# Kernel optimization log

Hardware: AMD Instinct MI355X
Metric: run time of the kernel (lower is better)

The kernel has to match this reference:

```python
import jax, jax.numpy as jnp
import numpy as np

NEG = -1e30  # safe "log zero" that avoids -inf - -inf = nan


def _segment_logsumexp(vals, seg, num_seg):
    # vals: [A] arc scores, seg: [A] destination state ids -> [num_seg]
    m = jax.ops.segment_max(vals, seg, num_segments=num_seg)
    m = jnp.maximum(m, NEG)  # empty segments give -inf
    s = jax.ops.segment_sum(jnp.exp(vals - m[seg]), seg, num_segments=num_seg)
    return m + jnp.log(s + 1e-30)


def setup_inputs() -> dict:
    key = jax.random.key(0)
    ks = jax.random.split(key, 7)
    T, B, D = 150, 64, 2048
    S, A = 20000, 262144
    inp = {
        "input": jax.nn.log_softmax(
            jax.random.normal(ks[0], (T, B, D), dtype=jnp.float32), axis=-1
        ),
        "arc_logw": 0.1 * jax.random.normal(ks[1], (A,), dtype=jnp.float32),
        "init_logp": jax.nn.log_softmax(
            jax.random.normal(ks[2], (S,), dtype=jnp.float32)
        ),
        "final_logp": 0.1 * jax.random.normal(ks[3], (S,), dtype=jnp.float32),
        "from_state": jax.random.randint(ks[4], (A,), 0, S, dtype=jnp.int32),
        "to_state": jax.random.randint(ks[5], (A,), 0, S, dtype=jnp.int32),
        "pdf_id": jax.random.randint(ks[6], (A,), 0, D, dtype=jnp.int32),
    }
    return inp


def reference(input, arc_logw, init_logp, final_logp, from_state, to_state, pdf_id):
    # LF-MMI denominator objective: log-semiring forward recursion over the
    # denominator WFST, summed over the batch.
    T, B, D = input.shape
    S = init_logp.shape[0]

    def step(alpha, logp_t):
        # alpha: [B, S] log forward probs; logp_t: [B, D] frame log-likelihoods
        # arc score = alpha[from] + arc weight + nnet logprob of arc's pdf
        scores = alpha[:, from_state] + arc_logw[None, :] + logp_t[:, pdf_id]  # [B, A]
        new_alpha = jax.vmap(lambda v: _segment_logsumexp(v, to_state, S))(scores)
        return new_alpha, None

    alpha0 = jnp.broadcast_to(init_logp[None, :], (B, S))
    alphaT, _ = jax.lax.scan(step, alpha0, input)  # scan over T frames
    per_seq = jax.scipy.special.logsumexp(alphaT + final_logp[None, :], axis=-1)  # [B]
    return jnp.sum(per_seq)
```

## Files before the change

### kernel.cpp

```cpp
#include <hip/hip_runtime.h>
#include <hip/hip_bf16.h>
#include <hip/hip_fp16.h>

#define NEGV (-1e30f)

constexpr int Bc = 64;
constexpr int Dc = 2048;
constexpr int Tc = 150;
constexpr float DRIFT = -5.0f;
constexpr float CLAMP_LO = -60.0f, CLAMP_HI = 40.0f;

__global__ void transpose_kernel(const float* __restrict__ in, __half* __restrict__ out) {
    __shared__ float tile[64][65];
    const int t  = blockIdx.y;
    const int d0 = blockIdx.x * 64;
    const int lane = threadIdx.x & 63;
    const int w    = threadIdx.x >> 6;
    const float* inp = in + (size_t)t * Bc * Dc;
    #pragma unroll
    for (int b = w; b < 64; b += 4)
        tile[b][lane] = inp[(size_t)b * Dc + d0 + lane];
    __syncthreads();
    __half* outp = out + (size_t)t * Dc * Bc;
    #pragma unroll
    for (int d = w; d < 64; d += 4)
        outp[(size_t)(d0 + d) * Bc + lane] = __float2half(tile[lane][d]);
}

__global__ void init_alpha_kernel(const float* __restrict__ init_logp,
                                  __half* __restrict__ alpha_h, int S) {
    int idx  = blockIdx.x * blockDim.x + threadIdx.x;
    int wave = idx >> 6;
    int lane = threadIdx.x & 63;
    if (wave < S) {
        float v = fminf(fmaxf(init_logp[wave], CLAMP_LO), CLAMP_HI);
        alpha_h[(size_t)wave * Bc + lane] = __float2half(v);
    }
}

__global__ void hist_kernel(const int* __restrict__ to, int* __restrict__ count, int A) {
    int i = blockIdx.x * blockDim.x + threadIdx.x;
    if (i < A) atomicAdd(&count[to[i]], 1);
}

__global__ void scan_kernel(const int* __restrict__ count, int* __restrict__ row_ptr,
                            int* __restrict__ cursor, int S) {
    __shared__ int lds[1024];
    const int tid = threadIdx.x;
    const int n = 1024;
    const int chunk = (S + n - 1) / n;
    const int lo = tid * chunk;
    const int hi = min(lo + chunk, S);
    int local = 0;
    for (int j = lo; j < hi; ++j) local += count[j];
    lds[tid] = local;
    __syncthreads();
    for (int off = 1; off < 1024; off <<= 1) {
        int add = (tid >= off) ? lds[tid - off] : 0;
        __syncthreads();
        lds[tid] += add;
        __syncthreads();
    }
    int excl = (tid > 0) ? lds[tid - 1] : 0;
    for (int j = lo; j < hi; ++j) {
        int c = count[j];
        row_ptr[j] = excl;
        cursor[j]  = excl;
        excl += c;
    }
    if (tid == n - 1) row_ptr[S] = lds[n - 1];
}

__global__ void scatter_kernel(const int* __restrict__ to, const int* __restrict__ from,
                               const int* __restrict__ pdf, const float* __restrict__ w,
                               int* __restrict__ cursor, uint2* __restrict__ a_pack, int A) {
    int i = blockIdx.x * blockDim.x + threadIdx.x;
    if (i >= A) return;
    int t = to[i];
    int p = atomicAdd(&cursor[t], 1);
    unsigned short wb = __half_as_ushort(__float2half(w[i]));
    a_pack[p] = make_uint2((unsigned)from[i],
                           ((unsigned)pdf[i] & 0xffffu) | ((unsigned)wb << 16));
}

template <bool TR>
__global__ void step_kernel(const __half* __restrict__ alpha_old,
                            __half* __restrict__ alpha_new,
                            const float* __restrict__ off_old,
                            float* __restrict__ off_new,
                            const void* __restrict__ logp_t,
                            const int* __restrict__ row_ptr,
                            const uint2* __restrict__ arcs, int S) {
    const int nb  = gridDim.x;
    const int cpx = nb >> 3;
    const int bid = blockIdx.x;
    const int swz = (nb % 8 == 0) ? ((bid & 7) * cpx + (bid >> 3)) : bid;
    const int wave = (swz * blockDim.x + threadIdx.x) >> 6;
    const int lane = threadIdx.x & 63;
    if (wave >= S) return;
    const int lo = __builtin_amdgcn_readfirstlane(row_ptr[wave]);
    const int hi = __builtin_amdgcn_readfirstlane(row_ptr[wave + 1]);
    const __half* lph = (const __half*)logp_t;
    const float*  lpf = (const float*)logp_t;

    const float r0 = __half2float(alpha_old[0 * Bc + lane]);
    const float r1 = __half2float(alpha_old[1 * Bc + lane]);
    const float r2 = __half2float(alpha_old[2 * Bc + lane]);
    const float r3 = __half2float(alpha_old[3 * Bc + lane]);
    const float delta = fmaxf(fmaxf(r0, r1), fmaxf(r2, r3)) + DRIFT;

    float s0 = 0.0f, s1 = 0.0f, s2 = 0.0f, s3 = 0.0f;
    int i = lo;
    for (; i + 3 < hi; i += 4) {
        const uint2 A0 = arcs[i],     A1 = arcs[i + 1];
        const uint2 A2 = arcs[i + 2], A3 = arcs[i + 3];
        const float w0 = __half2float(__ushort_as_half((unsigned short)(A0.y >> 16)));
        const float w1 = __half2float(__ushort_as_half((unsigned short)(A1.y >> 16)));
        const float w2 = __half2float(__ushort_as_half((unsigned short)(A2.y >> 16)));
        const float w3 = __half2float(__ushort_as_half((unsigned short)(A3.y >> 16)));
        const float lp0 = TR ? __half2float(lph[(size_t)(A0.y & 0xffffu) * Bc + lane])
                             : lpf[(size_t)lane * Dc + (A0.y & 0xffffu)];
        const float lp1 = TR ? __half2float(lph[(size_t)(A1.y & 0xffffu) * Bc + lane])
                             : lpf[(size_t)lane * Dc + (A1.y & 0xffffu)];
        const float lp2 = TR ? __half2float(lph[(size_t)(A2.y & 0xffffu) * Bc + lane])
                             : lpf[(size_t)lane * Dc + (A2.y & 0xffffu)];
        const float lp3 = TR ? __half2float(lph[(size_t)(A3.y & 0xffffu) * Bc + lane])
                             : lpf[(size_t)lane * Dc + (A3.y & 0xffffu)];
        const float a0 = __half2float(alpha_old[(size_t)A0.x * Bc + lane]);
        const float a1 = __half2float(alpha_old[(size_t)A1.x * Bc + lane]);
        const float a2 = __half2float(alpha_old[(size_t)A2.x * Bc + lane]);
        const float a3 = __half2float(alpha_old[(size_t)A3.x * Bc + lane]);
        s0 += __expf(a0 + w0 + lp0);
        s1 += __expf(a1 + w1 + lp1);
        s2 += __expf(a2 + w2 + lp2);
        s3 += __expf(a3 + w3 + lp3);
    }
    for (; i < hi; ++i) {
        const uint2 A0 = arcs[i];
        const float w0 = __half2float(__ushort_as_half((unsigned short)(A0.y >> 16)));
        const float lp0 = TR ? __half2float(lph[(size_t)(A0.y & 0xffffu) * Bc + lane])
                             : lpf[(size_t)lane * Dc + (A0.y & 0xffffu)];
        s0 += __expf(__half2float(alpha_old[(size_t)A0.x * Bc + lane]) + w0 + lp0);
    }
    const float r = __logf(((s0 + s1) + (s2 + s3)) + 1e-30f);
    const float v = fminf(fmaxf(r - delta, CLAMP_LO), CLAMP_HI);
    alpha_new[(size_t)wave * Bc + lane] = __float2half(v);
    if (wave == 0) off_new[lane] = off_old[lane] + delta;
}

__global__ void final_reduce_kernel(const __half* __restrict__ alpha,
                                    const float* __restrict__ off,
                                    const float* __restrict__ final_logp,
                                    float* __restrict__ out, int S) {
    const int b = blockIdx.x;
    const int tid = threadIdx.x;
    float m = NEGV, sum = 0.0f;
    for (int s = tid; s < S; s += 256) {
        float v = __half2float(alpha[(size_t)s * Bc + b]) + final_logp[s];
        float nm = fmaxf(m, v);
        sum = sum * __expf(m - nm) + __expf(v - nm);
        m = nm;
    }
    __shared__ float mArr[256], sArr[256];
    mArr[tid] = m; sArr[tid] = sum;
    __syncthreads();
    for (int o = 128; o > 0; o >>= 1) {
        if (tid < o) {
            float m2 = mArr[tid + o], s2 = sArr[tid + o];
            float nm = fmaxf(mArr[tid], m2);
            sArr[tid] = sArr[tid] * __expf(mArr[tid] - nm) + s2 * __expf(m2 - nm);
            mArr[tid] = nm;
        }
        __syncthreads();
    }
    if (tid == 0) {
        float per = fmaxf(mArr[0], NEGV) + logf(sArr[0] + 1e-30f) + off[b];
        atomicAdd(out, per);
    }
}

extern "C" void kernel_launch(void* const* d_in, const int* in_sizes, int n_in,
                              void* d_out, int out_size, void* d_ws, size_t ws_size,
                              hipStream_t stream) {
    const float* input      = (const float*)d_in[0];
    const float* arc_logw   = (const float*)d_in[1];
    const float* init_logp  = (const float*)d_in[2];
    const float* final_logp = (const float*)d_in[3];
    const int*   from_state = (const int*)d_in[4];
    const int*   to_state   = (const int*)d_in[5];
    const int*   pdf_id     = (const int*)d_in[6];
    const int S = in_sizes[2];
    const int A = in_sizes[4];

    char* ws = (char*)d_ws;
    size_t off = 0;
    auto alloc = [&](size_t bytes) -> char* {
        char* p = ws + off;
        off += (bytes + 255) & ~(size_t)255;
        return p;
    };

    const size_t need_small =
        2 * (((size_t)S * Bc * 2 + 255) & ~(size_t)255) +
        (((size_t)A * 8 + 255) & ~(size_t)255) +
        3 * (((size_t)(S + 1) * 4 + 255) & ~(size_t)255) +
        2 * 256;
    const size_t need_T = (size_t)Tc * Dc * Bc * 2 + 256;
    const bool do_transpose = (ws_size >= need_small + need_T);

    __half* logpT = nullptr;
    if (do_transpose) logpT = (__half*)alloc(need_T);
    __half* alphaA = (__half*)alloc((size_t)S * Bc * 2);
    __half* alphaB = (__half*)alloc((size_t)S * Bc * 2);
    float* offA    = (float*)alloc(Bc * 4);
    float* offB    = (float*)alloc(Bc * 4);
    int*   row_ptr = (int*)alloc((size_t)(S + 1) * 4);
    int*   cursor  = (int*)alloc((size_t)(S + 1) * 4);
    int*   count   = (int*)alloc((size_t)(S + 1) * 4);
    uint2* a_pack  = (uint2*)alloc((size_t)A * 8);

    hipMemsetAsync(count, 0, (size_t)S * 4, stream);
    hipMemsetAsync(offA, 0, Bc * 4, stream);
    hipMemsetAsync(d_out, 0, sizeof(float), stream);

    if (do_transpose) {
        dim3 tgrid(Dc / 64, Tc);
        transpose_kernel<<<tgrid, 256, 0, stream>>>(input, logpT);
    }
    init_alpha_kernel<<<(S * Bc + 255) / 256, 256, 0, stream>>>(init_logp, alphaA, S);
    hist_kernel<<<(A + 255) / 256, 256, 0, stream>>>(to_state, count, A);
    scan_kernel<<<1, 1024, 0, stream>>>(count, row_ptr, cursor, S);
    scatter_kernel<<<(A + 255) / 256, 256, 0, stream>>>(to_state, from_state, pdf_id,
                                                        arc_logw, cursor, a_pack, A);

    __half* curA = alphaA;  __half* nxtA = alphaB;
    float*  curO = offA;    float*  nxtO = offB;
    int step_blocks = (S + 3) / 4;
    step_blocks = (step_blocks + 7) & ~7;
    for (int t = 0; t < Tc; ++t) {
        if (do_transpose) {
            step_kernel<true><<<step_blocks, 256, 0, stream>>>(
                curA, nxtA, curO, nxtO, logpT + (size_t)t * Dc * Bc, row_ptr, a_pack, S);
        } else {
            step_kernel<false><<<step_blocks, 256, 0, stream>>>(
                curA, nxtA, curO, nxtO, input + (size_t)t * Bc * Dc, row_ptr, a_pack, S);
        }
        __half* ta = curA; curA = nxtA; nxtA = ta;
        float*  to_ = curO; curO = nxtO; nxtO = to_;
    }
    final_reduce_kernel<<<Bc, 256, 0, stream>>>(curA, curO, final_logp, (float*)d_out, S);
}
```

Before: 2.060 ms.

## Switch forward recursion from log domain to scaled linear probability domain

Alpha, arc weights and frame likelihoods are now stored as exponentiated values with a per-frame rescale, so each arc costs a multiply-add instead of an expf, and the per-state logf is gone. The weight and likelihood exponentials are computed once in the setup kernels (scatter, transpose), and a running log offset per sequence tracks the scale. The step kernel also moves to 512-thread blocks. The risk is fp16 range: linear-domain values can underflow to zero, and the scale comes only from alpha of states 0-3, which may not track the true maximum.

Measured after the change: 2.017 ms, median of 3. 1.02x faster.

```diff
diff --git a/kernel.cpp b/kernel.cpp
--- a/kernel.cpp
+++ b/kernel.cpp
@@ -7,8 +7,9 @@
 constexpr int Bc = 64;
 constexpr int Dc = 2048;
 constexpr int Tc = 150;
-constexpr float DRIFT = -5.0f;
-constexpr float CLAMP_LO = -60.0f, CLAMP_HI = 40.0f;
+constexpr float EXP_NEG_DRIFT = 148.41316f;
+constexpr float STORE_CAP = 60000.0f;
+constexpr float OFF_INIT = -10.0f;
 
 __global__ void transpose_kernel(const float* __restrict__ in, __half* __restrict__ out) {
     __shared__ float tile[64][65];
@@ -24,18 +25,20 @@
     __half* outp = out + (size_t)t * Dc * Bc;
     #pragma unroll
     for (int d = w; d < 64; d += 4)
-        outp[(size_t)(d0 + d) * Bc + lane] = __float2half(tile[lane][d]);
+        outp[(size_t)(d0 + d) * Bc + lane] = __float2half(__expf(tile[lane][d]));
 }
 
 __global__ void init_alpha_kernel(const float* __restrict__ init_logp,
-                                  __half* __restrict__ alpha_h, int S) {
+                                  __half* __restrict__ alpha_h,
+                                  float* __restrict__ off, int S) {
     int idx  = blockIdx.x * blockDim.x + threadIdx.x;
     int wave = idx >> 6;
     int lane = threadIdx.x & 63;
     if (wave < S) {
-        float v = fminf(fmaxf(init_logp[wave], CLAMP_LO), CLAMP_HI);
-        alpha_h[(size_t)wave * Bc + lane] = __float2half(v);
-    }
+        float v = __expf(init_logp[wave] - OFF_INIT);
+        alpha_h[(size_t)wave * Bc + lane] = __float2half(fminf(v, STORE_CAP));
+    }
+    if (idx < Bc) off[idx] = OFF_INIT;
 }
 
 __global__ void hist_kernel(const int* __restrict__ to, int* __restrict__ count, int A) {
@@ -78,7 +81,7 @@
     if (i >= A) return;
     int t = to[i];
     int p = atomicAdd(&cursor[t], 1);
-    unsigned short wb = __half_as_ushort(__float2half(w[i]));
+    unsigned short wb = __half_as_ushort(__float2half(__expf(w[i])));
     a_pack[p] = make_uint2((unsigned)from[i],
                            ((unsigned)pdf[i] & 0xffffu) | ((unsigned)wb << 16));
 }
@@ -107,7 +110,8 @@
     const float r1 = __half2float(alpha_old[1 * Bc + lane]);
     const float r2 = __half2float(alpha_old[2 * Bc + lane]);
     const float r3 = __half2float(alpha_old[3 * Bc + lane]);
-    const float delta = fmaxf(fmaxf(r0, r1), fmaxf(r2, r3)) + DRIFT;
+    const float dref = fmaxf(fmaxf(fmaxf(r0, r1), fmaxf(r2, r3)), 1e-20f);
+    const float scale = EXP_NEG_DRIFT / dref;
 
     float s0 = 0.0f, s1 = 0.0f, s2 = 0.0f, s3 = 0.0f;
     int i = lo;
@@ -118,34 +122,34 @@
         const float w1 = __half2float(__ushort_as_half((unsigned short)(A1.y >> 16)));
         const float w2 = __half2float(__ushort_as_half((unsigned short)(A2.y >> 16)));
         const float w3 = __half2float(__ushort_as_half((unsigned short)(A3.y >> 16)));
-        const float lp0 = TR ? __half2float(lph[(size_t)(A0.y & 0xffffu) * Bc + lane])
-                             : lpf[(size_t)lane * Dc + (A0.y & 0xffffu)];
-        const float lp1 = TR ? __half2float(lph[(size_t)(A1.y & 0xffffu) * Bc + lane])
-                             : lpf[(size_t)lane * Dc + (A1.y & 0xffffu)];
-        const float lp2 = TR ? __half2float(lph[(size_t)(A2.y & 0xffffu) * Bc + lane])
-                             : lpf[(size_t)lane * Dc + (A2.y & 0xffffu)];
-        const float lp3 = TR ? __half2float(lph[(size_t)(A3.y & 0xffffu) * Bc + lane])
-                             : lpf[(size_t)lane * Dc + (A3.y & 0xffffu)];
+        const float e0 = TR ? __half2float(lph[(size_t)(A0.y & 0xffffu) * Bc + lane])
+                            : __expf(lpf[(size_t)lane * Dc + (A0.y & 0xffffu)]);
+        const float e1 = TR ? __half2float(lph[(size_t)(A1.y & 0xffffu) * Bc + lane])
+                            : __expf(lpf[(size_t)lane * Dc + (A1.y & 0xffffu)]);
+        const float e2 = TR ? __half2float(lph[(size_t)(A2.y & 0xffffu) * Bc + lane])
+                            : __expf(lpf[(size_t)lane * Dc + (A2.y & 0xffffu)]);
+        const float e3 = TR ? __half2float(lph[(size_t)(A3.y & 0xffffu) * Bc + lane])
+                            : __expf(lpf[(size_t)lane * Dc + (A3.y & 0xffffu)]);
         const float a0 = __half2float(alpha_old[(size_t)A0.x * Bc + lane]);
         const float a1 = __half2float(alpha_old[(size_t)A1.x * Bc + lane]);
         const float a2 = __half2float(alpha_old[(size_t)A2.x * Bc + lane]);
         const float a3 = __half2float(alpha_old[(size_t)A3.x * Bc + lane]);
-        s0 += __expf(a0 + w0 + lp0);
-        s1 += __expf(a1 + w1 + lp1);
-        s2 += __expf(a2 + w2 + lp2);
-        s3 += __expf(a3 + w3 + lp3);
+        s0 = fmaf(a0 * w0, e0, s0);
+        s1 = fmaf(a1 * w1, e1, s1);
+        s2 = fmaf(a2 * w2, e2, s2);
+        s3 = fmaf(a3 * w3, e3, s3);
     }
     for (; i < hi; ++i) {
         const uint2 A0 = arcs[i];
         const float w0 = __half2float(__ushort_as_half((unsigned short)(A0.y >> 16)));
-        const float lp0 = TR ? __half2float(lph[(size_t)(A0.y & 0xffffu) * Bc + lane])
-                             : lpf[(size_t)lane * Dc + (A0.y & 0xffffu)];
-        s0 += __expf(__half2float(alpha_old[(size_t)A0.x * Bc + lane]) + w0 + lp0);
-    }
-    const float r = __logf(((s0 + s1) + (s2 + s3)) + 1e-30f);
-    const float v = fminf(fmaxf(r - delta, CLAMP_LO), CLAMP_HI);
-    alpha_new[(size_t)wave * Bc + lane] = __float2half(v);
-    if (wave == 0) off_new[lane] = off_old[lane] + delta;
+        const float e0 = TR ? __half2float(lph[(size_t)(A0.y & 0xffffu) * Bc + lane])
+                            : __expf(lpf[(size_t)lane * Dc + (A0.y & 0xffffu)]);
+        const float a0 = __half2float(alpha_old[(size_t)A0.x * Bc + lane]);
+        s0 = fmaf(a0 * w0, e0, s0);
+    }
+    const float s = (s0 + s1) + (s2 + s3);
+    alpha_new[(size_t)wave * Bc + lane] = __float2half(fminf(s * scale, STORE_CAP));
+    if (wave == 0) off_new[lane] = off_old[lane] + (__logf(dref) - 5.0f);
 }
 
 __global__ void final_reduce_kernel(const __half* __restrict__ alpha,
@@ -156,7 +160,8 @@
     const int tid = threadIdx.x;
     float m = NEGV, sum = 0.0f;
     for (int s = tid; s < S; s += 256) {
-        float v = __half2float(alpha[(size_t)s * Bc + b]) + final_logp[s];
+        float ea = __half2float(alpha[(size_t)s * Bc + b]);
+        float v = __logf(ea + 1e-35f) + final_logp[s];
         float nm = fmaxf(m, v);
         sum = sum * __expf(m - nm) + __expf(v - nm);
         m = nm;
@@ -220,14 +225,14 @@
     uint2* a_pack  = (uint2*)alloc((size_t)A * 8);
 
     hipMemsetAsync(count, 0, (size_t)S * 4, stream);
-    hipMemsetAsync(offA, 0, Bc * 4, stream);
     hipMemsetAsync(d_out, 0, sizeof(float), stream);
 
     if (do_transpose) {
         dim3 tgrid(Dc / 64, Tc);
         transpose_kernel<<<tgrid, 256, 0, stream>>>(input, logpT);
     }
-    init_alpha_kernel<<<(S * Bc + 255) / 256, 256, 0, stream>>>(init_logp, alphaA, S);
+    init_alpha_kernel<<<(S * Bc + 255) / 256, 256, 0, stream>>>(init_logp, alphaA,
+                                                                offA, S);
     hist_kernel<<<(A + 255) / 256, 256, 0, stream>>>(to_state, count, A);
     scan_kernel<<<1, 1024, 0, stream>>>(count, row_ptr, cursor, S);
     scatter_kernel<<<(A + 255) / 256, 256, 0, stream>>>(to_state, from_state, pdf_id,
@@ -235,14 +240,14 @@
 
     __half* curA = alphaA;  __half* nxtA = alphaB;
     float*  curO = offA;    float*  nxtO = offB;
-    int step_blocks = (S + 3) / 4;
+    int step_blocks = (S + 7) / 8;
     step_blocks = (step_blocks + 7) & ~7;
     for (int t = 0; t < Tc; ++t) {
         if (do_transpose) {
-            step_kernel<true><<<step_blocks, 256, 0, stream>>>(
+            step_kernel<true><<<step_blocks, 512, 0, stream>>>(
                 curA, nxtA, curO, nxtO, logpT + (size_t)t * Dc * Bc, row_ptr, a_pack, S);
         } else {
-            step_kernel<false><<<step_blocks, 256, 0, stream>>>(
+            step_kernel<false><<<step_blocks, 512, 0, stream>>>(
                 curA, nxtA, curO, nxtO, input + (size_t)t * Bc * Dc, row_ptr, a_pack, S);
         }
         __half* ta = curA; curA = nxtA; nxtA = ta;
```
